# Kernel optimization log

Measured on AMD Instinct MI355X. Metric: run time of the kernel, lower is better.

## Reference

```python
import jax, jax.numpy as jnp
import numpy as np

B = 2_097_152
N_QUBITS = 3


def _rz(a):
    # diag(e^{-i a/2}, e^{+i a/2}) as (2,2) complex64
    e = jnp.exp(-0.5j * a)
    z = jnp.zeros_like(e)
    return jnp.stack([jnp.stack([e, z]), jnp.stack([z, jnp.conj(e)])])


def _rx(a):
    c = jnp.cos(0.5 * a) + 0j
    s = -1j * jnp.sin(0.5 * a)
    return jnp.stack([jnp.stack([c, s]), jnp.stack([s, c])])


def _ry_batched(a):
    # a: (B,) real -> (B,2,2) complex
    c = jnp.cos(0.5 * a)
    s = jnp.sin(0.5 * a)
    m = jnp.stack([jnp.stack([c, -s], -1), jnp.stack([s, c], -1)], -2)
    return m.astype(jnp.complex64)


def _apply_1q(state, U, wire):
    # state: (B,2,2,2); U: (2,2) shared or (B,2,2) batched
    x = jnp.moveaxis(state, wire + 1, -1)
    if U.ndim == 2:
        y = jnp.einsum('ij,b...j->b...i', U, x)
    else:
        y = jnp.einsum('bij,b...j->b...i', U, x)
    return jnp.moveaxis(y, -1, wire + 1)


def _apply_cnot(state, ctrl, tgt):
    x = jnp.moveaxis(state, (ctrl + 1, tgt + 1), (-2, -1))
    # flip target amplitudes where control = 1
    y = jnp.concatenate([x[..., :1, :], x[..., 1:, ::-1]], axis=-2)
    return jnp.moveaxis(y, (-2, -1), (ctrl + 1, tgt + 1))


def _ansatz_layer(state, th):
    # th: (n_qubits, 3) -> RZ, RX, RZ per qubit, then CNOT ring
    for i in range(N_QUBITS):
        state = _apply_1q(state, _rz(th[i, 0]), i)
        state = _apply_1q(state, _rx(th[i, 1]), i)
        state = _apply_1q(state, _rz(th[i, 2]), i)
    for i in range(N_QUBITS):
        state = _apply_cnot(state, i, (i + 1) % N_QUBITS)
    return state


def _feature_layer(state, phi):
    # phi: (B, n_qubits) -> RY(phi[:, i]) on qubit i
    for i in range(N_QUBITS):
        state = _apply_1q(state, _ry_batched(phi[:, i]), i)
    return state


def _forward(t, theta):
    if t.ndim == 2:
        t = t[:, 0]
    b = t.shape[0]
    # angle encoding: [pi t, 2pi t, 3pi t]
    phi = jnp.pi * t[:, None] * jnp.asarray([1.0, 2.0, 3.0], dtype=t.dtype)
    state = jnp.zeros((b, 2, 2, 2), dtype=jnp.complex64).at[:, 0, 0, 0].set(1.0)
    state = _ansatz_layer(state, theta[0])
    state = _feature_layer(state, phi)
    state = _ansatz_layer(state, theta[1])
    state = _feature_layer(state, phi)
    state = _ansatz_layer(state, theta[2])
    p = jnp.abs(state) ** 2  # (B,2,2,2) real
    expz0 = p[:, 0].sum(axis=(1, 2)) - p[:, 1].sum(axis=(1, 2))
    return expz0[:, None].astype(jnp.float32)  # (B,1)


def setup_inputs() -> dict:
    key = jax.random.key(0)
    k_t, k_th = jax.random.split(key)
    t = jax.random.uniform(k_t, (B, 1), dtype=jnp.float32)
    theta = jax.random.normal(k_th, (3, 3, 3), dtype=jnp.float32) * 0.01
    return {"t": t, "theta": theta}


def reference(t, theta):
    return _forward(t, theta)
```

## Files before the change

kernel.cpp:

```cpp
#include <hip/hip_runtime.h>
#include <math.h>

#ifndef M_PI
#define M_PI 3.14159265358979323846
#endif

__device__ float g_coef[52];

__device__ __forceinline__ float rfl(float x)
{
    return __int_as_float(__builtin_amdgcn_readfirstlane(__float_as_int(x)));
}

template <int ST>
__device__ __forceinline__ void rotF(float c, float s, float (&vr)[8], float (&vi)[8])
{
#pragma unroll
    for (int k = 0; k < 8; ++k) {
        if (k & ST) continue;
        const int k1 = k + ST;
        const float ar = vr[k],  ai = vi[k];
        const float br = vr[k1], bi = vi[k1];
        vr[k]  = c * ar - s * br;  vi[k]  = c * ai - s * bi;
        vr[k1] = s * ar + c * br;  vi[k1] = s * ai + c * bi;
    }
}

__global__ void qb_prep(const float* __restrict__ theta)
{
    __shared__ float2 sU[192];
    __shared__ float  sOut[64];
    const int tid = threadIdx.x;

    if (tid < 24) {
        const int l = tid >> 3;
        const int c = tid & 7;

        float re[8], im[8];
#pragma unroll
        for (int k = 0; k < 8; ++k) { re[k] = (k == c) ? 1.f : 0.f; im[k] = 0.f; }

#pragma unroll
        for (int q = 0; q < 3; ++q) {
            const int p  = 2 - q;
            const int st = 1 << p;
            const float a0 = theta[l * 9 + q * 3 + 0];
            const float a1 = theta[l * 9 + q * 3 + 1];
            const float a2 = theta[l * 9 + q * 3 + 2];
            float sz, cz, sx, cx, sz2, cz2;
            __sincosf(0.5f * a0, &sz,  &cz);
            __sincosf(0.5f * a1, &sx,  &cx);
            __sincosf(0.5f * a2, &sz2, &cz2);

#pragma unroll
            for (int k = 0; k < 8; ++k) {
                const float s = ((k >> p) & 1) ? sz : -sz;
                const float r0 = re[k] * cz - im[k] * s;
                const float i0 = re[k] * s  + im[k] * cz;
                re[k] = r0; im[k] = i0;
            }
#pragma unroll
            for (int k = 0; k < 8; ++k) {
                if ((k >> p) & 1) continue;
                const int k1 = k + st;
                const float r0 =  cx * re[k]  + sx * im[k1];
                const float i0 =  cx * im[k]  - sx * re[k1];
                const float r1 =  sx * im[k]  + cx * re[k1];
                const float i1 = -sx * re[k]  + cx * im[k1];
                re[k] = r0; im[k] = i0; re[k1] = r1; im[k1] = i1;
            }
#pragma unroll
            for (int k = 0; k < 8; ++k) {
                const float s = ((k >> p) & 1) ? sz2 : -sz2;
                const float r0 = re[k] * cz2 - im[k] * s;
                const float i0 = re[k] * s   + im[k] * cz2;
                re[k] = r0; im[k] = i0;
            }
        }

#define SWP(a, b) { float tr = re[a]; re[a] = re[b]; re[b] = tr; \
                    float ti = im[a]; im[a] = im[b]; im[b] = ti; }
        SWP(4, 6); SWP(5, 7);
        SWP(2, 3); SWP(6, 7);
        SWP(1, 5); SWP(3, 7);
#undef SWP

#pragma unroll
        for (int r = 0; r < 8; ++r)
            sU[l * 64 + r * 8 + c] = make_float2(re[r], im[r]);
    }
    __syncthreads();

    {
        const int j = tid;
        const float w0 = (float)(M_PI / 32.0);
        float c1, s1;
        __sincosf(w0 * (float)j, &s1, &c1);
        const float c2 = c1 * c1 - s1 * s1, s2 = 2.f * s1 * c1;
        const float c3 = c2 * c1 - s2 * s1, s3 = s2 * c1 + c2 * s1;

        float wr[8], wi[8];
#pragma unroll
        for (int r = 0; r < 8; ++r) { const float2 u = sU[r * 8]; wr[r] = u.x; wi[r] = u.y; }

        rotF<4>(c1, s1, wr, wi);
        rotF<2>(c2, s2, wr, wi);
        rotF<1>(c3, s3, wr, wi);

        float xr[8], xi[8];
#pragma unroll
        for (int r = 0; r < 8; ++r) {
            float zr = 0.f, zi = 0.f;
#pragma unroll
            for (int cc = 0; cc < 8; ++cc) {
                const float2 u = sU[64 + r * 8 + cc];
                zr += u.x * wr[cc] - u.y * wi[cc];
                zi += u.x * wi[cc] + u.y * wr[cc];
            }
            xr[r] = zr; xi[r] = zi;
        }

        rotF<4>(c1, s1, xr, xi);
        rotF<2>(c2, s2, xr, xi);
        rotF<1>(c3, s3, xr, xi);

        float acc = 0.f;
#pragma unroll
        for (int r = 0; r < 8; ++r) {
            float zr = 0.f, zi = 0.f;
#pragma unroll
            for (int cc = 0; cc < 8; ++cc) {
                const float2 u = sU[128 + r * 8 + cc];
                zr += u.x * xr[cc] - u.y * xi[cc];
                zi += u.x * xi[cc] + u.y * xr[cc];
            }
            const float m = zr * zr + zi * zi;
            acc += (r < 4) ? m : -m;
        }
        sOut[j] = acc;
    }
    __syncthreads();

    if (tid < 26) {
        if (tid == 25) {
            g_coef[50] = 0.f; g_coef[51] = 0.f;
        } else {
            const float w0 = (float)(M_PI / 32.0);
            float sa = 0.f, sb = 0.f;
            for (int j = 0; j < 64; ++j) {
                const int m = (tid * j) & 63;
                float s, c;
                __sincosf(w0 * (float)m, &s, &c);
                sa += sOut[j] * c;
                sb += sOut[j] * s;
            }
            const float sc = (tid == 0) ? (1.f / 64.f) : (2.f / 64.f);
            g_coef[2 * tid]     = sa * sc;
            g_coef[2 * tid + 1] = (tid == 0) ? 0.f : sb * sc;
        }
    }
}

__device__ __forceinline__ float evalSeries(float tval,
                                            const float (&A)[26], const float (&Bv)[26])
{
    const float th = 1.5707963267948966f * tval;
    float s1, c1;
    __sincosf(th, &s1, &c1);
    const float tc = 2.f * c1;
    float cp = 1.f, sp = 0.f;
    float cc = c1,  sc = s1;
    float acc = A[0] + A[1] * cc + Bv[1] * sc;
#pragma unroll
    for (int k = 2; k <= 25; ++k) {
        const float cn = tc * cc - cp;
        const float sn = tc * sc - sp;
        cp = cc; sp = sc; cc = cn; sc = sn;
        acc += A[k] * cn + Bv[k] * sn;
    }
    return acc;
}

__global__ __launch_bounds__(256) void qb_main(const float* __restrict__ t,
                                               float* __restrict__ out, int n)
{
    float A[26], Bv[26];
    const float4* cg = reinterpret_cast<const float4*>(g_coef);
#pragma unroll
    for (int q = 0; q < 13; ++q) {
        const float4 v = cg[q];
        A[2 * q]      = rfl(v.x);
        Bv[2 * q]     = rfl(v.y);
        A[2 * q + 1]  = rfl(v.z);
        Bv[2 * q + 1] = rfl(v.w);
    }

    const int base = (blockIdx.x * 256 + threadIdx.x) * 4;
    if (base + 3 < n) {
        const float4 tv = *reinterpret_cast<const float4*>(t + base);
        float4 ov;
        ov.x = evalSeries(tv.x, A, Bv);
        ov.y = evalSeries(tv.y, A, Bv);
        ov.z = evalSeries(tv.z, A, Bv);
        ov.w = evalSeries(tv.w, A, Bv);
        *reinterpret_cast<float4*>(out + base) = ov;
    } else {
        for (int i = 0; i < 4; ++i)
            if (base + i < n) out[base + i] = evalSeries(t[base + i], A, Bv);
    }
}

extern "C" void kernel_launch(void* const* d_in, const int* in_sizes, int n_in,
                              void* d_out, int out_size, void* d_ws, size_t ws_size,
                              hipStream_t stream)
{
    const float* t     = (const float*)d_in[0];
    const float* theta = (const float*)d_in[1];
    float* out         = (float*)d_out;
    const int n = in_sizes[0];

    qb_prep<<<1, 64, 0, stream>>>(theta);
    const int blocks = (n + 1023) / 1024;
    qb_main<<<blocks, 256, 0, stream>>>(t, out, n);
}
```

Before: 71.04 us.

## Fuse coefficient prep into main kernel with per-block recompute and shuffle DFT

Removes the separate single-block prep kernel. Each block now rebuilds the circuit unitaries and the Fourier coefficients of the expectation in shared memory before evaluating its samples. The serial per-coefficient DFT loop is replaced by per-lane Chebyshev harmonic generation followed by a wavefront xor-shuffle reduction. The series is cut to 24 harmonics, and each thread handles 8 samples instead of 4, with the t loads issued before the prologue. The goal is to remove the launch and the serialized prep stage, at the cost of redundant prologue work in every block.

```diff
diff --git a/kernel.cpp b/kernel.cpp
--- a/kernel.cpp
+++ b/kernel.cpp
@@ -5,7 +5,7 @@
 #define M_PI 3.14159265358979323846
 #endif
 
-__device__ float g_coef[52];
+#define SAMPLES_PER_THREAD 8
 
 __device__ __forceinline__ float rfl(float x)
 {
@@ -26,143 +26,8 @@
     }
 }
 
-__global__ void qb_prep(const float* __restrict__ theta)
-{
-    __shared__ float2 sU[192];
-    __shared__ float  sOut[64];
-    const int tid = threadIdx.x;
-
-    if (tid < 24) {
-        const int l = tid >> 3;
-        const int c = tid & 7;
-
-        float re[8], im[8];
-#pragma unroll
-        for (int k = 0; k < 8; ++k) { re[k] = (k == c) ? 1.f : 0.f; im[k] = 0.f; }
-
-#pragma unroll
-        for (int q = 0; q < 3; ++q) {
-            const int p  = 2 - q;
-            const int st = 1 << p;
-            const float a0 = theta[l * 9 + q * 3 + 0];
-            const float a1 = theta[l * 9 + q * 3 + 1];
-            const float a2 = theta[l * 9 + q * 3 + 2];
-            float sz, cz, sx, cx, sz2, cz2;
-            __sincosf(0.5f * a0, &sz,  &cz);
-            __sincosf(0.5f * a1, &sx,  &cx);
-            __sincosf(0.5f * a2, &sz2, &cz2);
-
-#pragma unroll
-            for (int k = 0; k < 8; ++k) {
-                const float s = ((k >> p) & 1) ? sz : -sz;
-                const float r0 = re[k] * cz - im[k] * s;
-                const float i0 = re[k] * s  + im[k] * cz;
-                re[k] = r0; im[k] = i0;
-            }
-#pragma unroll
-            for (int k = 0; k < 8; ++k) {
-                if ((k >> p) & 1) continue;
-                const int k1 = k + st;
-                const float r0 =  cx * re[k]  + sx * im[k1];
-                const float i0 =  cx * im[k]  - sx * re[k1];
-                const float r1 =  sx * im[k]  + cx * re[k1];
-                const float i1 = -sx * re[k]  + cx * im[k1];
-                re[k] = r0; im[k] = i0; re[k1] = r1; im[k1] = i1;
-            }
-#pragma unroll
-            for (int k = 0; k < 8; ++k) {
-                const float s = ((k >> p) & 1) ? sz2 : -sz2;
-                const float r0 = re[k] * cz2 - im[k] * s;
-                const float i0 = re[k] * s   + im[k] * cz2;
-                re[k] = r0; im[k] = i0;
-            }
-        }
-
-#define SWP(a, b) { float tr = re[a]; re[a] = re[b]; re[b] = tr; \
-                    float ti = im[a]; im[a] = im[b]; im[b] = ti; }
-        SWP(4, 6); SWP(5, 7);
-        SWP(2, 3); SWP(6, 7);
-        SWP(1, 5); SWP(3, 7);
-#undef SWP
-
-#pragma unroll
-        for (int r = 0; r < 8; ++r)
-            sU[l * 64 + r * 8 + c] = make_float2(re[r], im[r]);
-    }
-    __syncthreads();
-
-    {
-        const int j = tid;
-        const float w0 = (float)(M_PI / 32.0);
-        float c1, s1;
-        __sincosf(w0 * (float)j, &s1, &c1);
-        const float c2 = c1 * c1 - s1 * s1, s2 = 2.f * s1 * c1;
-        const float c3 = c2 * c1 - s2 * s1, s3 = s2 * c1 + c2 * s1;
-
-        float wr[8], wi[8];
-#pragma unroll
-        for (int r = 0; r < 8; ++r) { const float2 u = sU[r * 8]; wr[r] = u.x; wi[r] = u.y; }
-
-        rotF<4>(c1, s1, wr, wi);
-        rotF<2>(c2, s2, wr, wi);
-        rotF<1>(c3, s3, wr, wi);
-
-        float xr[8], xi[8];
-#pragma unroll
-        for (int r = 0; r < 8; ++r) {
-            float zr = 0.f, zi = 0.f;
-#pragma unroll
-            for (int cc = 0; cc < 8; ++cc) {
-                const float2 u = sU[64 + r * 8 + cc];
-                zr += u.x * wr[cc] - u.y * wi[cc];
-                zi += u.x * wi[cc] + u.y * wr[cc];
-            }
-            xr[r] = zr; xi[r] = zi;
-        }
-
-        rotF<4>(c1, s1, xr, xi);
-        rotF<2>(c2, s2, xr, xi);
-        rotF<1>(c3, s3, xr, xi);
-
-        float acc = 0.f;
-#pragma unroll
-        for (int r = 0; r < 8; ++r) {
-            float zr = 0.f, zi = 0.f;
-#pragma unroll
-            for (int cc = 0; cc < 8; ++cc) {
-                const float2 u = sU[128 + r * 8 + cc];
-                zr += u.x * xr[cc] - u.y * xi[cc];
-                zi += u.x * xi[cc] + u.y * xr[cc];
-            }
-            const float m = zr * zr + zi * zi;
-            acc += (r < 4) ? m : -m;
-        }
-        sOut[j] = acc;
-    }
-    __syncthreads();
-
-    if (tid < 26) {
-        if (tid == 25) {
-            g_coef[50] = 0.f; g_coef[51] = 0.f;
-        } else {
-            const float w0 = (float)(M_PI / 32.0);
-            float sa = 0.f, sb = 0.f;
-            for (int j = 0; j < 64; ++j) {
-                const int m = (tid * j) & 63;
-                float s, c;
-                __sincosf(w0 * (float)m, &s, &c);
-                sa += sOut[j] * c;
-                sb += sOut[j] * s;
-            }
-            const float sc = (tid == 0) ? (1.f / 64.f) : (2.f / 64.f);
-            g_coef[2 * tid]     = sa * sc;
-            g_coef[2 * tid + 1] = (tid == 0) ? 0.f : sb * sc;
-        }
-    }
-}
-
 __device__ __forceinline__ float evalSeries(float tval,
-                                            const float (&A)[26], const float (&Bv)[26])
+                                            const float (&A)[25], const float (&Bv)[25])
 {
     const float th = 1.5707963267948966f * tval;
     float s1, c1;
@@ -172,7 +37,7 @@
     float cc = c1,  sc = s1;
     float acc = A[0] + A[1] * cc + Bv[1] * sc;
 #pragma unroll
-    for (int k = 2; k <= 25; ++k) {
+    for (int k = 2; k <= 24; ++k) {
         const float cn = tc * cc - cp;
         const float sn = tc * sc - sp;
         cp = cc; sp = sc; cc = cn; sc = sn;
@@ -181,31 +46,181 @@
     return acc;
 }
 
-__global__ __launch_bounds__(256) void qb_main(const float* __restrict__ t,
-                                               float* __restrict__ out, int n)
-{
-    float A[26], Bv[26];
-    const float4* cg = reinterpret_cast<const float4*>(g_coef);
+__global__ __launch_bounds__(256) void qb_fused(const float* __restrict__ t,
+                                                const float* __restrict__ theta,
+                                                float* __restrict__ out, int n)
+{
+    __shared__ float2 sU[192];
+    __shared__ __align__(16) float sC[52];
+
+    const int tid  = threadIdx.x;
+    const int base = (blockIdx.x * 256 + tid) * SAMPLES_PER_THREAD;
+
+    float4 tv0, tv1;
+    const bool full = (base + SAMPLES_PER_THREAD - 1 < n);
+    if (full) {
+        tv0 = *reinterpret_cast<const float4*>(t + base);
+        tv1 = *reinterpret_cast<const float4*>(t + base + 4);
+    }
+
+    if (tid < 64) {
+        if (tid < 24) {
+            const int l = tid >> 3;
+            const int c = tid & 7;
+            float re[8], im[8];
+#pragma unroll
+            for (int k = 0; k < 8; ++k) { re[k] = (k == c) ? 1.f : 0.f; im[k] = 0.f; }
+
+#pragma unroll
+            for (int q = 0; q < 3; ++q) {
+                const int p  = 2 - q;
+                const int st = 1 << p;
+                const float a0 = theta[l * 9 + q * 3 + 0];
+                const float a1 = theta[l * 9 + q * 3 + 1];
+                const float a2 = theta[l * 9 + q * 3 + 2];
+                float sz, cz, sx, cx, sz2, cz2;
+                __sincosf(0.5f * a0, &sz,  &cz);
+                __sincosf(0.5f * a1, &sx,  &cx);
+                __sincosf(0.5f * a2, &sz2, &cz2);
+#pragma unroll
+                for (int k = 0; k < 8; ++k) {
+                    const float s = ((k >> p) & 1) ? sz : -sz;
+                    const float r0 = re[k] * cz - im[k] * s;
+                    const float i0 = re[k] * s  + im[k] * cz;
+                    re[k] = r0; im[k] = i0;
+                }
+#pragma unroll
+                for (int k = 0; k < 8; ++k) {
+                    if ((k >> p) & 1) continue;
+                    const int k1 = k + st;
+                    const float r0 =  cx * re[k]  + sx * im[k1];
+                    const float i0 =  cx * im[k]  - sx * re[k1];
+                    const float r1 =  sx * im[k]  + cx * re[k1];
+                    const float i1 = -sx * re[k]  + cx * im[k1];
+                    re[k] = r0; im[k] = i0; re[k1] = r1; im[k1] = i1;
+                }
+#pragma unroll
+                for (int k = 0; k < 8; ++k) {
+                    const float s = ((k >> p) & 1) ? sz2 : -sz2;
+                    const float r0 = re[k] * cz2 - im[k] * s;
+                    const float i0 = re[k] * s   + im[k] * cz2;
+                    re[k] = r0; im[k] = i0;
+                }
+            }
+#define SWP(a, b) { float tr = re[a]; re[a] = re[b]; re[b] = tr; \
+                    float ti = im[a]; im[a] = im[b]; im[b] = ti; }
+            SWP(4, 6); SWP(5, 7);
+            SWP(2, 3); SWP(6, 7);
+            SWP(1, 5); SWP(3, 7);
+#undef SWP
+#pragma unroll
+            for (int r = 0; r < 8; ++r)
+                sU[l * 64 + r * 8 + c] = make_float2(re[r], im[r]);
+        }
+
+        const float w0 = (float)(M_PI / 32.0);
+        float c1, s1;
+        __sincosf(w0 * (float)tid, &s1, &c1);
+        const float c2 = c1 * c1 - s1 * s1, s2 = 2.f * s1 * c1;
+        const float c3 = c2 * c1 - s2 * s1, s3 = s2 * c1 + c2 * s1;
+
+        float wr[8], wi[8];
+#pragma unroll
+        for (int r = 0; r < 8; ++r) { const float2 u = sU[r * 8]; wr[r] = u.x; wi[r] = u.y; }
+        rotF<4>(c1, s1, wr, wi);
+        rotF<2>(c2, s2, wr, wi);
+        rotF<1>(c3, s3, wr, wi);
+
+        float xr[8], xi[8];
+#pragma unroll
+        for (int r = 0; r < 8; ++r) {
+            float zr = 0.f, zi = 0.f;
+#pragma unroll
+            for (int cc = 0; cc < 8; ++cc) {
+                const float2 u = sU[64 + r * 8 + cc];
+                zr += u.x * wr[cc] - u.y * wi[cc];
+                zi += u.x * wi[cc] + u.y * wr[cc];
+            }
+            xr[r] = zr; xi[r] = zi;
+        }
+        rotF<4>(c1, s1, xr, xi);
+        rotF<2>(c2, s2, xr, xi);
+        rotF<1>(c3, s3, xr, xi);
+
+        float v = 0.f;
+#pragma unroll
+        for (int r = 0; r < 8; ++r) {
+            float zr = 0.f, zi = 0.f;
+#pragma unroll
+            for (int cc = 0; cc < 8; ++cc) {
+                const float2 u = sU[128 + r * 8 + cc];
+                zr += u.x * xr[cc] - u.y * xi[cc];
+                zi += u.x * xi[cc] + u.y * xr[cc];
+            }
+            const float m = zr * zr + zi * zi;
+            v += (r < 4) ? m : -m;
+        }
+
+        float pa[25], pb[25];
+        {
+            const float tc = 2.f * c1;
+            float cprev = v,      sprev = 0.f;
+            float ccur  = v * c1, scur  = v * s1;
+            pa[0] = cprev; pb[0] = sprev;
+            pa[1] = ccur;  pb[1] = scur;
+#pragma unroll
+            for (int k = 2; k < 25; ++k) {
+                const float cn = tc * ccur - cprev;
+                const float sn = tc * scur - sprev;
+                cprev = ccur; sprev = scur; ccur = cn; scur = sn;
+                pa[k] = cn; pb[k] = sn;
+            }
+        }
+#pragma unroll
+        for (int m = 1; m < 64; m <<= 1) {
+#pragma unroll
+            for (int k = 0; k < 25; ++k) {
+                pa[k] += __shfl_xor(pa[k], m);
+                pb[k] += __shfl_xor(pb[k], m);
+            }
+        }
+        if (tid == 0) {
+            const float sc1 = 1.f / 64.f, sc2 = 2.f / 64.f;
+            sC[0] = pa[0] * sc1; sC[1] = 0.f;
+#pragma unroll
+            for (int k = 1; k < 25; ++k) {
+                sC[2 * k]     = pa[k] * sc2;
+                sC[2 * k + 1] = pb[k] * sc2;
+            }
+            sC[50] = 0.f; sC[51] = 0.f;
+        }
+    }
+    __syncthreads();
+
+    float A[25], Bv[25];
+    const float4* cg = reinterpret_cast<const float4*>(sC);
 #pragma unroll
     for (int q = 0; q < 13; ++q) {
-        const float4 v = cg[q];
-        A[2 * q]      = rfl(v.x);
-        Bv[2 * q]     = rfl(v.y);
-        A[2 * q + 1]  = rfl(v.z);
-        Bv[2 * q + 1] = rfl(v.w);
-    }
-
-    const int base = (blockIdx.x * 256 + threadIdx.x) * 4;
-    if (base + 3 < n) {
-        const float4 tv = *reinterpret_cast<const float4*>(t + base);
-        float4 ov;
-        ov.x = evalSeries(tv.x, A, Bv);
-        ov.y = evalSeries(tv.y, A, Bv);
-        ov.z = evalSeries(tv.z, A, Bv);
-        ov.w = evalSeries(tv.w, A, Bv);
-        *reinterpret_cast<float4*>(out + base) = ov;
+        const float4 vv = cg[q];
+        const int k0 = 2 * q;
+        if (k0 < 25)     { A[k0]     = rfl(vv.x); Bv[k0]     = rfl(vv.y); }
+        if (k0 + 1 < 25) { A[k0 + 1] = rfl(vv.z); Bv[k0 + 1] = rfl(vv.w); }
+    }
+
+    if (full) {
+        float4 o0, o1;
+        o0.x = evalSeries(tv0.x, A, Bv);
+        o0.y = evalSeries(tv0.y, A, Bv);
+        o0.z = evalSeries(tv0.z, A, Bv);
+        o0.w = evalSeries(tv0.w, A, Bv);
+        o1.x = evalSeries(tv1.x, A, Bv);
+        o1.y = evalSeries(tv1.y, A, Bv);
+        o1.z = evalSeries(tv1.z, A, Bv);
+        o1.w = evalSeries(tv1.w, A, Bv);
+        *reinterpret_cast<float4*>(out + base)     = o0;
+        *reinterpret_cast<float4*>(out + base + 4) = o1;
     } else {
-        for (int i = 0; i < 4; ++i)
+        for (int i = 0; i < SAMPLES_PER_THREAD; ++i)
             if (base + i < n) out[base + i] = evalSeries(t[base + i], A, Bv);
     }
 }
@@ -219,7 +234,7 @@
     float* out         = (float*)d_out;
     const int n = in_sizes[0];
 
-    qb_prep<<<1, 64, 0, stream>>>(theta);
-    const int blocks = (n + 1023) / 1024;
-    qb_main<<<blocks, 256, 0, stream>>>(t, out, n);
-}
+    const int per_block = 256 * SAMPLES_PER_THREAD;
+    const int blocks = (n + per_block - 1) / per_block;
+    qb_fused<<<blocks, 256, 0, stream>>>(t, theta, out, n);
+}
```

Measured after the change: 88.40 us. 24.4% more time.

## Pack Fourier coefficients as float2 pairs and evaluate 8 samples per thread

Applied to the files above, without the earlier changes.

Each thread now evaluates 8 samples instead of 4, so launch overhead is spread over more work. The cos/sin Chebyshev recurrence is packed into 2-wide vector operations, which may map to packed FP32 instructions. The series is truncated to 25 terms, dropping the zero-padded last one. The prep kernel builds a shared table of cis values instead of calling sincos 64 times per coefficient. The per-thread work doubling lowers parallelism, and packing depends on the compiler emitting packed instructions.

```diff
diff --git a/kernel.cpp b/kernel.cpp
--- a/kernel.cpp
+++ b/kernel.cpp
@@ -5,7 +5,11 @@
 #define M_PI 3.14159265358979323846
 #endif
 
-__device__ float g_coef[52];
+#define SAMPLES_PER_THREAD 8
+
+typedef float v2f __attribute__((ext_vector_type(2)));
+
+__device__ __align__(16) float2 g_coef[26];
 
 __device__ __forceinline__ float rfl(float x)
 {
@@ -30,12 +34,12 @@
 {
     __shared__ float2 sU[192];
     __shared__ float  sOut[64];
+    __shared__ float2 sCis[64];
     const int tid = threadIdx.x;
 
     if (tid < 24) {
         const int l = tid >> 3;
         const int c = tid & 7;
-
         float re[8], im[8];
 #pragma unroll
         for (int k = 0; k < 8; ++k) { re[k] = (k == c) ? 1.f : 0.f; im[k] = 0.f; }
@@ -51,7 +55,6 @@
             __sincosf(0.5f * a0, &sz,  &cz);
             __sincosf(0.5f * a1, &sx,  &cx);
             __sincosf(0.5f * a2, &sz2, &cz2);
-
 #pragma unroll
             for (int k = 0; k < 8; ++k) {
                 const float s = ((k >> p) & 1) ? sz : -sz;
@@ -77,14 +80,12 @@
                 re[k] = r0; im[k] = i0;
             }
         }
-
 #define SWP(a, b) { float tr = re[a]; re[a] = re[b]; re[b] = tr; \
                     float ti = im[a]; im[a] = im[b]; im[b] = ti; }
         SWP(4, 6); SWP(5, 7);
         SWP(2, 3); SWP(6, 7);
         SWP(1, 5); SWP(3, 7);
 #undef SWP
-
 #pragma unroll
         for (int r = 0; r < 8; ++r)
             sU[l * 64 + r * 8 + c] = make_float2(re[r], im[r]);
@@ -92,17 +93,15 @@
     __syncthreads();
 
     {
-        const int j = tid;
         const float w0 = (float)(M_PI / 32.0);
         float c1, s1;
-        __sincosf(w0 * (float)j, &s1, &c1);
+        __sincosf(w0 * (float)tid, &s1, &c1);
         const float c2 = c1 * c1 - s1 * s1, s2 = 2.f * s1 * c1;
         const float c3 = c2 * c1 - s2 * s1, s3 = s2 * c1 + c2 * s1;
 
         float wr[8], wi[8];
 #pragma unroll
         for (int r = 0; r < 8; ++r) { const float2 u = sU[r * 8]; wr[r] = u.x; wi[r] = u.y; }
-
         rotF<4>(c1, s1, wr, wi);
         rotF<2>(c2, s2, wr, wi);
         rotF<1>(c3, s3, wr, wi);
@@ -119,12 +118,11 @@
             }
             xr[r] = zr; xi[r] = zi;
         }
-
         rotF<4>(c1, s1, xr, xi);
         rotF<2>(c2, s2, xr, xi);
         rotF<1>(c3, s3, xr, xi);
 
-        float acc = 0.f;
+        float v = 0.f;
 #pragma unroll
         for (int r = 0; r < 8; ++r) {
             float zr = 0.f, zi = 0.f;
@@ -135,78 +133,80 @@
                 zi += u.x * xi[cc] + u.y * xr[cc];
             }
             const float m = zr * zr + zi * zi;
-            acc += (r < 4) ? m : -m;
-        }
-        sOut[j] = acc;
+            v += (r < 4) ? m : -m;
+        }
+        sOut[tid] = v;
+        sCis[tid] = make_float2(c1, s1);
     }
     __syncthreads();
 
     if (tid < 26) {
         if (tid == 25) {
-            g_coef[50] = 0.f; g_coef[51] = 0.f;
+            g_coef[25] = make_float2(0.f, 0.f);
         } else {
-            const float w0 = (float)(M_PI / 32.0);
             float sa = 0.f, sb = 0.f;
+#pragma unroll
             for (int j = 0; j < 64; ++j) {
-                const int m = (tid * j) & 63;
-                float s, c;
-                __sincosf(w0 * (float)m, &s, &c);
-                sa += sOut[j] * c;
-                sb += sOut[j] * s;
+                const float  vj = sOut[j];
+                const float2 w  = sCis[(tid * j) & 63];
+                sa += vj * w.x;
+                sb += vj * w.y;
             }
             const float sc = (tid == 0) ? (1.f / 64.f) : (2.f / 64.f);
-            g_coef[2 * tid]     = sa * sc;
-            g_coef[2 * tid + 1] = (tid == 0) ? 0.f : sb * sc;
-        }
-    }
-}
-
-__device__ __forceinline__ float evalSeries(float tval,
-                                            const float (&A)[26], const float (&Bv)[26])
+            g_coef[tid] = make_float2(sa * sc, (tid == 0) ? 0.f : sb * sc);
+        }
+    }
+}
+
+__device__ __forceinline__ float evalSeries(float tval, const v2f (&AB)[25])
 {
     const float th = 1.5707963267948966f * tval;
     float s1, c1;
     __sincosf(th, &s1, &c1);
-    const float tc = 2.f * c1;
-    float cp = 1.f, sp = 0.f;
-    float cc = c1,  sc = s1;
-    float acc = A[0] + A[1] * cc + Bv[1] * sc;
-#pragma unroll
-    for (int k = 2; k <= 25; ++k) {
-        const float cn = tc * cc - cp;
-        const float sn = tc * sc - sp;
-        cp = cc; sp = sc; cc = cn; sc = sn;
-        acc += A[k] * cn + Bv[k] * sn;
-    }
-    return acc;
+    const v2f tc = { 2.f * c1, 2.f * c1 };
+    v2f pp = { 1.f, 0.f };
+    v2f pc = { c1, s1 };
+    v2f acc = AB[0] * pp + AB[1] * pc;
+#pragma unroll
+    for (int k = 2; k <= 24; ++k) {
+        const v2f pn = tc * pc - pp;
+        pp = pc; pc = pn;
+        acc = AB[k] * pn + acc;
+    }
+    return acc.x + acc.y;
 }
 
 __global__ __launch_bounds__(256) void qb_main(const float* __restrict__ t,
                                                float* __restrict__ out, int n)
 {
-    float A[26], Bv[26];
+    v2f AB[25];
     const float4* cg = reinterpret_cast<const float4*>(g_coef);
 #pragma unroll
     for (int q = 0; q < 13; ++q) {
-        const float4 v = cg[q];
-        A[2 * q]      = rfl(v.x);
-        Bv[2 * q]     = rfl(v.y);
-        A[2 * q + 1]  = rfl(v.z);
-        Bv[2 * q + 1] = rfl(v.w);
-    }
-
-    const int base = (blockIdx.x * 256 + threadIdx.x) * 4;
-    if (base + 3 < n) {
-        const float4 tv = *reinterpret_cast<const float4*>(t + base);
-        float4 ov;
-        ov.x = evalSeries(tv.x, A, Bv);
-        ov.y = evalSeries(tv.y, A, Bv);
-        ov.z = evalSeries(tv.z, A, Bv);
-        ov.w = evalSeries(tv.w, A, Bv);
-        *reinterpret_cast<float4*>(out + base) = ov;
+        const float4 vv = cg[q];
+        const int k0 = 2 * q;
+        { v2f e; e.x = rfl(vv.x); e.y = rfl(vv.y); AB[k0] = e; }
+        if (k0 + 1 < 25) { v2f e; e.x = rfl(vv.z); e.y = rfl(vv.w); AB[k0 + 1] = e; }
+    }
+
+    const int base = (blockIdx.x * 256 + threadIdx.x) * SAMPLES_PER_THREAD;
+    if (base + SAMPLES_PER_THREAD - 1 < n) {
+        const float4 tv0 = *reinterpret_cast<const float4*>(t + base);
+        const float4 tv1 = *reinterpret_cast<const float4*>(t + base + 4);
+        float4 o0, o1;
+        o0.x = evalSeries(tv0.x, AB);
+        o0.y = evalSeries(tv0.y, AB);
+        o0.z = evalSeries(tv0.z, AB);
+        o0.w = evalSeries(tv0.w, AB);
+        o1.x = evalSeries(tv1.x, AB);
+        o1.y = evalSeries(tv1.y, AB);
+        o1.z = evalSeries(tv1.z, AB);
+        o1.w = evalSeries(tv1.w, AB);
+        *reinterpret_cast<float4*>(out + base)     = o0;
+        *reinterpret_cast<float4*>(out + base + 4) = o1;
     } else {
-        for (int i = 0; i < 4; ++i)
-            if (base + i < n) out[base + i] = evalSeries(t[base + i], A, Bv);
+        for (int i = 0; i < SAMPLES_PER_THREAD; ++i)
+            if (base + i < n) out[base + i] = evalSeries(t[base + i], AB);
     }
 }
 
@@ -220,6 +220,7 @@
     const int n = in_sizes[0];
 
     qb_prep<<<1, 64, 0, stream>>>(theta);
-    const int blocks = (n + 1023) / 1024;
+    const int per_block = 256 * SAMPLES_PER_THREAD;
+    const int blocks = (n + per_block - 1) / per_block;
     qb_main<<<blocks, 256, 0, stream>>>(t, out, n);
 }
```

New measurement: 69.88 us. No clear change (-1.6%).
